# Performance work log

Hardware: AMD Instinct MI355X
Metric: run time of the kernel (lower is better)

Reference implementation:

```python
import jax, jax.numpy as jnp
from jax import lax
import numpy as np

B, S, W, Dw, Dc, F, K, Dt, P, H, T, BL = 16, 256, 16, 300, 50, 128, 3, 768, 256, 128, 9, 384
VW, VC = 100000, 128


def setup_inputs():
    ks = jax.random.split(jax.random.key(0), 32)
    f = lambda i, shape, s=0.05: jax.random.normal(ks[i], shape, dtype=jnp.float32) * s
    inp = {
        'words': jax.random.randint(ks[0], (B, S), 0, VW, dtype=jnp.int32),
        'chars': jax.random.randint(ks[1], (B, S, W), 0, VC, dtype=jnp.int32),
        'tags': jax.random.randint(ks[2], (B, S), 0, T, dtype=jnp.int32),
        'word_mask': jnp.ones((B, S), dtype=bool),
        'word_maps': jax.random.randint(ks[3], (B, S), 0, BL, dtype=jnp.int32),
        'bert_hidden': jax.random.normal(ks[4], (B, BL, Dt), dtype=jnp.float32),
        'w2v_table': f(5, (VW, Dw)).at[0].set(0.0),   # padding_idx=0
        'char_table': f(6, (VC, Dc)).at[0].set(0.0),  # padding_idx=0
        'conv_w': f(7, (F, Dc, K)), 'conv_b': f(8, (F,)),
        'w2v_pw': f(9, (Dw, P)), 'w2v_pb': f(10, (P,)),
        'char_pw': f(11, (F, P)), 'char_pb': f(12, (P,)),
        'trans_pw': f(13, (Dt, P)), 'trans_pb': f(14, (P,)),
        'attn_pw': f(15, (P, P // 2)), 'attn_pb': f(16, (P // 2,)),
        'attn_sw': f(17, (P // 2, 1)), 'attn_sb': f(18, (1,)),
        'lf_wih': f(19, (P, 4 * H)), 'lf_whh': f(20, (H, 4 * H)), 'lf_b': f(21, (4 * H,)),
        'lb_wih': f(22, (P, 4 * H)), 'lb_whh': f(23, (H, 4 * H)), 'lb_b': f(24, (4 * H,)),
        'h2t_w': f(25, (2 * H, T)), 'h2t_b': f(26, (T,)),
        'crf_start': f(27, (T,)), 'crf_end': f(28, (T,)), 'crf_trans': f(29, (T, T)),
    }
    return inp


def _lstm_dir(x, wih, whh, b, reverse):
    # x: [B,S,D]; pytorch gate order i,f,g,o; h0=c0=0
    Bx = x.shape[0]
    Hh = whh.shape[0]
    pre = jnp.einsum('bsd,dg->sbg', x, wih) + b  # [S,B,4H]
    if reverse:
        pre = pre[::-1]

    def step(carry, g):
        h, c = carry
        g = g + h @ whh
        i, f_, gg, o = jnp.split(g, 4, axis=-1)
        c = jax.nn.sigmoid(f_) * c + jax.nn.sigmoid(i) * jnp.tanh(gg)
        h = jax.nn.sigmoid(o) * jnp.tanh(c)
        return (h, c), h

    h0 = jnp.zeros((Bx, Hh), x.dtype)
    _, hs = lax.scan(step, (h0, h0), pre)
    if reverse:
        hs = hs[::-1]
    return hs.transpose(1, 0, 2)  # [B,S,H]


def _crf_loglik(emissions, tags, mask, start, end, trans):
    # torchcrf log-likelihood, batch_first inputs transposed to time-major
    Bx = emissions.shape[0]
    em = emissions.transpose(1, 0, 2)          # [S,B,T]
    tg = tags.T                                 # [S,B]
    mk = mask.T.astype(emissions.dtype)         # [S,B]
    bidx = jnp.arange(Bx)

    # numerator: score of gold path
    score0 = start[tg[0]] + em[0, bidx, tg[0]]

    def num_step(carry, x):
        score, prev = carry
        e, t, m = x
        score = score + (trans[prev, t] + e[bidx, t]) * m
        prev = jnp.where(m > 0, t, prev)
        return (score, prev), None

    (score, last_tag), _ = lax.scan(num_step, (score0, tg[0]), (em[1:], tg[1:], mk[1:]))
    numerator = score + end[last_tag]

    # denominator: forward algorithm (log-sum-exp scan)
    alpha0 = start[None, :] + em[0]

    def den_step(alpha, x):
        e, m = x
        nxt = jax.scipy.special.logsumexp(alpha[:, :, None] + trans[None] + e[:, None, :], axis=1)
        return jnp.where(m[:, None] > 0, nxt, alpha), None

    alpha, _ = lax.scan(den_step, alpha0, (em[1:], mk[1:]))
    denominator = jax.scipy.special.logsumexp(alpha + end[None, :], axis=1)
    return numerator - denominator


def reference(words, chars, tags, word_mask, word_maps, bert_hidden,
              w2v_table, char_table, conv_w, conv_b,
              w2v_pw, w2v_pb, char_pw, char_pb, trans_pw, trans_pb,
              attn_pw, attn_pb, attn_sw, attn_sb,
              lf_wih, lf_whh, lf_b, lb_wih, lb_whh, lb_b,
              h2t_w, h2t_b, crf_start, crf_end, crf_trans):
    Bx, Sx = words.shape
    w2v = w2v_table[words]                                   # [B,S,Dw]
    # CharCNN: embed -> conv1d (same pad) -> max over word_len
    ce = char_table[chars]                                   # [B,S,W,Dc]
    x = ce.reshape(Bx * Sx, ce.shape[2], ce.shape[3]).transpose(0, 2, 1)  # [BS,Dc,W]
    k = conv_w.shape[-1]
    c = lax.conv_general_dilated(x, conv_w, (1,), [(k // 2, k // 2)],
                                 dimension_numbers=('NCW', 'OIW', 'NCW'))
    c = c + conv_b[None, :, None]
    char_feat = c.max(axis=2).reshape(Bx, Sx, -1)            # [B,S,F]
    # gather subword states to word positions (vectorized word_maps double-loop)
    tf = jnp.take_along_axis(bert_hidden, word_maps[:, :, None], axis=1)  # [B,S,Dt]
    p1 = jax.nn.relu(w2v @ w2v_pw + w2v_pb)
    p2 = jax.nn.relu(char_feat @ char_pw + char_pb)
    p3 = jax.nn.relu(tf @ trans_pw + trans_pb)
    stacked = jnp.stack([p1, p2, p3], axis=2)                # [B,S,3,P]
    proj = jnp.tanh(stacked @ attn_pw + attn_pb)
    scores = (proj @ attn_sw + attn_sb)[..., 0]              # [B,S,3]
    wts = jax.nn.softmax(scores, axis=2)
    fused = (wts[..., None] * stacked).sum(axis=2)           # [B,S,P]
    hf = _lstm_dir(fused, lf_wih, lf_whh, lf_b, False)
    hb = _lstm_dir(fused, lb_wih, lb_whh, lb_b, True)
    lstm_out = jnp.concatenate([hf, hb], axis=-1)            # [B,S,2H]
    emissions = lstm_out @ h2t_w + h2t_b                     # [B,S,T]
    llh = _crf_loglik(emissions, tags, word_mask, crf_start, crf_end, crf_trans)
    return -llh.mean()
```

## Files before the change

### kernel.cpp

```cpp
#include <hip/hip_runtime.h>
#include <math.h>

#define BB   16
#define SS   256
#define WWID 16
#define DW   300
#define DC   50
#define FF   128
#define DT   768
#define PP   256
#define HH   128
#define TT   9
#define BLL  384
#define NTOK (BB*SS)

__device__ __forceinline__ float sigmoidf_(float x){ return 1.f/(1.f+expf(-x)); }
__device__ __forceinline__ float fsig_(float x){ return __frcp_rn(1.f + __expf(-x)); }
__device__ __forceinline__ float ftanh_(float x){ return 1.f - 2.f*__frcp_rn(__expf(2.f*x) + 1.f); }

__global__ void k_charconv(const int* __restrict__ chars,
                           const float* __restrict__ char_table,
                           const float* __restrict__ conv_w,
                           const float* __restrict__ conv_b,
                           float* __restrict__ char_feat){
  __shared__ __align__(16) float sm_ce[WWID][DC];
  const int tok = blockIdx.x;
  const int tid = threadIdx.x;
  for (int idx = tid; idx < WWID*DC; idx += 128){
    int w = idx / DC, c = idx - w*DC;
    sm_ce[w][c] = char_table[chars[tok*WWID + w]*DC + c];
  }
  __syncthreads();
  const int f = tid;
  float acc[WWID];
  const float bias = conv_b[f];
  #pragma unroll
  for (int w = 0; w < WWID; w++) acc[w] = bias;
  const float* cw = conv_w + f*DC*3;
  for (int c = 0; c < DC; c++){
    float w0 = cw[c*3+0], w1 = cw[c*3+1], w2 = cw[c*3+2];
    float xm = 0.f, x0 = sm_ce[0][c];
    #pragma unroll
    for (int w = 0; w < WWID; w++){
      float xp = (w < WWID-1) ? sm_ce[w+1][c] : 0.f;
      acc[w] += xm*w0 + x0*w1 + xp*w2;
      xm = x0; x0 = xp;
    }
  }
  float mx = acc[0];
  #pragma unroll
  for (int w = 1; w < WWID; w++) mx = fmaxf(mx, acc[w]);
  char_feat[tok*FF + f] = mx;
}

__global__ void k_proj(const int* __restrict__ words,
                       const int* __restrict__ word_maps,
                       const float* __restrict__ w2v_table,
                       const float* __restrict__ bert,
                       const float* __restrict__ char_feat,
                       const float* __restrict__ w2v_pw, const float* __restrict__ w2v_pb,
                       const float* __restrict__ char_pw, const float* __restrict__ char_pb,
                       const float* __restrict__ trans_pw, const float* __restrict__ trans_pb,
                       float* __restrict__ stacked){
  const int MT = 16;
  __shared__ __align__(16) float sm_x[MT*128];
  const int bx  = blockIdx.x;
  const int src = bx >> 8;
  const int m0  = (bx & 255) * MT;
  const int tid = threadIdx.x;
  const int Ksz = (src==0) ? DW : (src==1 ? FF : DT);
  const float* Wt = (src==0) ? w2v_pw : (src==1 ? char_pw : trans_pw);
  const float* bv = (src==0) ? w2v_pb : (src==1 ? char_pb : trans_pb);

  float acc[MT];
  #pragma unroll
  for (int m = 0; m < MT; m++) acc[m] = 0.f;

  for (int kc = 0; kc < Ksz; kc += 128){
    const int kk = min(128, Ksz - kc);
    for (int m = 0; m < MT; m++){
      const int tok = m0 + m;
      for (int k = tid; k < kk; k += 256){
        float v;
        if (src == 0)      v = w2v_table[(long)words[tok]*DW + kc + k];
        else if (src == 1) v = char_feat[tok*FF + kc + k];
        else               v = bert[((long)(tok>>8)*BLL + word_maps[tok])*DT + kc + k];
        sm_x[m*128 + k] = v;
      }
    }
    __syncthreads();
    const int k4 = kk & ~3;
    for (int k = 0; k < k4; k += 4){
      const float wv0 = Wt[(kc+k+0)*PP + tid];
      const float wv1 = Wt[(kc+k+1)*PP + tid];
      const float wv2 = Wt[(kc+k+2)*PP + tid];
      const float wv3 = Wt[(kc+k+3)*PP + tid];
      #pragma unroll
      for (int m = 0; m < MT; m++){
        const float4 x = *reinterpret_cast<const float4*>(&sm_x[m*128 + k]);
        acc[m] += x.x*wv0 + x.y*wv1 + x.z*wv2 + x.w*wv3;
      }
    }
    for (int k = k4; k < kk; k++){
      const float wv = Wt[(kc+k)*PP + tid];
      #pragma unroll
      for (int m = 0; m < MT; m++) acc[m] += sm_x[m*128 + k]*wv;
    }
    __syncthreads();
  }
  const float b0 = bv[tid];
  for (int m = 0; m < MT; m++){
    const float v = fmaxf(acc[m] + b0, 0.f);
    stacked[((long)(m0+m)*3 + src)*PP + tid] = v;
  }
}

__global__ void k_attn(const float* __restrict__ stacked,
                       const float* __restrict__ attn_pw, const float* __restrict__ attn_pb,
                       const float* __restrict__ attn_sw, const float* __restrict__ attn_sb,
                       float* __restrict__ fused){
  const int MT = 4;
  __shared__ __align__(16) float sm_st[MT*3*PP];
  __shared__ float sm_prod[MT*3*128];
  __shared__ float sm_sc[MT*3];
  __shared__ float sm_w[MT][3];
  const int m0  = blockIdx.x * MT;
  const int tid = threadIdx.x;
  for (int idx = tid; idx < MT*3*PP; idx += 256)
    sm_st[idx] = stacked[(long)m0*3*PP + idx];
  __syncthreads();
  for (int task = tid; task < MT*3*128; task += 256){
    const int i = task / 384;
    const int r = task - i*384;
    const int j = r >> 7;
    const int q = r & 127;
    const float* xv = &sm_st[(i*3 + j)*PP];
    float acc = attn_pb[q];
    for (int p = 0; p < PP; p += 4){
      const float4 x = *reinterpret_cast<const float4*>(&xv[p]);
      acc += x.x*attn_pw[(p+0)*128+q] + x.y*attn_pw[(p+1)*128+q]
           + x.z*attn_pw[(p+2)*128+q] + x.w*attn_pw[(p+3)*128+q];
    }
    sm_prod[task] = tanhf(acc) * attn_sw[q];
  }
  __syncthreads();
  if (tid < MT*3){
    const int i = tid/3, j = tid - i*3;
    float s = attn_sb[0];
    for (int q = 0; q < 128; q++) s += sm_prod[(i*3 + j)*128 + q];
    sm_sc[tid] = s;
  }
  __syncthreads();
  if (tid < MT){
    const float a = sm_sc[tid*3], b = sm_sc[tid*3+1], c = sm_sc[tid*3+2];
    const float m = fmaxf(a, fmaxf(b, c));
    const float ea = expf(a-m), eb = expf(b-m), ec = expf(c-m);
    const float inv = 1.f/(ea+eb+ec);
    sm_w[tid][0] = ea*inv; sm_w[tid][1] = eb*inv; sm_w[tid][2] = ec*inv;
  }
  __syncthreads();
  for (int idx = tid; idx < MT*PP; idx += 256){
    const int i = idx >> 8, p = idx & 255;
    const float v = sm_w[i][0]*sm_st[(i*3+0)*PP+p]
                  + sm_w[i][1]*sm_st[(i*3+1)*PP+p]
                  + sm_w[i][2]*sm_st[(i*3+2)*PP+p];
    fused[(long)(m0+i)*PP + p] = v;
  }
}

__global__ void k_pre(const float* __restrict__ fused,
                      const float* __restrict__ lf_wih, const float* __restrict__ lf_b,
                      const float* __restrict__ lb_wih, const float* __restrict__ lb_b,
                      float* __restrict__ pre_f, float* __restrict__ pre_b){
  const int MT = 8;
  __shared__ __align__(16) float sm_f[MT*PP];
  const int m0  = blockIdx.x * MT;
  const int tid = threadIdx.x;
  for (int idx = tid; idx < MT*PP; idx += 512) sm_f[idx] = fused[(long)m0*PP + idx];
  __syncthreads();
  float af[MT], ab[MT];
  #pragma unroll
  for (int m = 0; m < MT; m++){ af[m] = 0.f; ab[m] = 0.f; }
  for (int k = 0; k < PP; k += 4){
    const float wf0 = lf_wih[(k+0)*512 + tid];
    const float wf1 = lf_wih[(k+1)*512 + tid];
    const float wf2 = lf_wih[(k+2)*512 + tid];
    const float wf3 = lf_wih[(k+3)*512 + tid];
    const float wb0 = lb_wih[(k+0)*512 + tid];
    const float wb1 = lb_wih[(k+1)*512 + tid];
    const float wb2 = lb_wih[(k+2)*512 + tid];
    const float wb3 = lb_wih[(k+3)*512 + tid];
    #pragma unroll
    for (int m = 0; m < MT; m++){
      const float4 x = *reinterpret_cast<const float4*>(&sm_f[m*PP + k]);
      af[m] += x.x*wf0 + x.y*wf1 + x.z*wf2 + x.w*wf3;
      ab[m] += x.x*wb0 + x.y*wb1 + x.z*wb2 + x.w*wb3;
    }
  }
  const float bf = lf_b[tid], bbv = lb_b[tid];
  for (int m = 0; m < MT; m++){
    pre_f[(long)(m0+m)*512 + tid] = af[m] + bf;
    pre_b[(long)(m0+m)*512 + tid] = ab[m] + bbv;
  }
}

#define LDW(i) float4 W##i; \
  W##i.x = wcol[(4*(i)+0)*512]; W##i.y = wcol[(4*(i)+1)*512]; \
  W##i.z = wcol[(4*(i)+2)*512]; W##i.w = wcol[(4*(i)+3)*512];
#define FMW(i) { const float4 h4 = *reinterpret_cast<const float4*>(&sm_h[4*(i)]); \
  g0 = fmaf(h4.x, W##i.x, g0); g1 = fmaf(h4.y, W##i.y, g1); \
  g2 = fmaf(h4.z, W##i.z, g2); g3 = fmaf(h4.w, W##i.w, g3); }

__global__ void __launch_bounds__(512, 1)
k_lstm(const float* __restrict__ pre_f, const float* __restrict__ pre_b,
       const float* __restrict__ lf_whh, const float* __restrict__ lb_whh,
       float* __restrict__ lstm_out){
  __shared__ __align__(16) float sm_h[HH];
  __shared__ __align__(16) float sm_g[512];
  const int b = blockIdx.x & 15;
  const int d = blockIdx.x >> 4;
  const float* pre = d ? pre_b : pre_f;
  const float* whh = d ? lb_whh : lf_whh;
  const int tid = threadIdx.x;

  const float* wcol = whh + tid;
  LDW(0)  LDW(1)  LDW(2)  LDW(3)  LDW(4)  LDW(5)  LDW(6)  LDW(7)
  LDW(8)  LDW(9)  LDW(10) LDW(11) LDW(12) LDW(13) LDW(14) LDW(15)
  LDW(16) LDW(17) LDW(18) LDW(19) LDW(20) LDW(21) LDW(22) LDW(23)
  LDW(24) LDW(25) LDW(26) LDW(27) LDW(28) LDW(29) LDW(30) LDW(31)

  float c = 0.f;
  if (tid < HH) sm_h[tid] = 0.f;
  __syncthreads();

  const long step = d ? -512 : 512;
  const float* pp = pre + ((long)b*SS + (d ? SS-1 : 0))*512 + tid;
  float pcur = *pp;

  for (int s = 0; s < SS; s++){
    const int ss = d ? (SS-1-s) : s;
    pp += step;
    float pnext = (s+1 < SS) ? *pp : 0.f;
    float g0 = pcur, g1 = 0.f, g2 = 0.f, g3 = 0.f;
    FMW(0)  FMW(1)  FMW(2)  FMW(3)  FMW(4)  FMW(5)  FMW(6)  FMW(7)
    FMW(8)  FMW(9)  FMW(10) FMW(11) FMW(12) FMW(13) FMW(14) FMW(15)
    FMW(16) FMW(17) FMW(18) FMW(19) FMW(20) FMW(21) FMW(22) FMW(23)
    FMW(24) FMW(25) FMW(26) FMW(27) FMW(28) FMW(29) FMW(30) FMW(31)
    sm_g[tid] = (g0+g1)+(g2+g3);
    __syncthreads();
    if (tid < HH){
      const float iv = fsig_(sm_g[tid]);
      const float fv = fsig_(sm_g[HH + tid]);
      const float gv = ftanh_(sm_g[2*HH + tid]);
      const float ov = fsig_(sm_g[3*HH + tid]);
      c = fv*c + iv*gv;
      const float h = ov*ftanh_(c);
      sm_h[tid] = h;
      lstm_out[((long)b*SS + ss)*(2*HH) + d*HH + tid] = h;
    }
    __syncthreads();
    pcur = pnext;
  }
}

__global__ void k_emis(const float* __restrict__ lstm_out,
                       const float* __restrict__ h2t_w, const float* __restrict__ h2t_b,
                       float* __restrict__ emis){
  const int idx = blockIdx.x*blockDim.x + threadIdx.x;
  if (idx >= NTOK*TT) return;
  const int tok = idx / TT, t = idx - tok*TT;
  float acc = h2t_b[t];
  const float* x = &lstm_out[(long)tok*256];
  for (int k = 0; k < 256; k++) acc += x[k]*h2t_w[k*TT + t];
  emis[idx] = acc;
}

__global__ void k_crf(const float* __restrict__ emis, const int* __restrict__ tags,
                      const float* __restrict__ startv, const float* __restrict__ endv,
                      const float* __restrict__ trans, float* __restrict__ out){
  __shared__ float sm_part[256];
  __shared__ float sm_num[BB];
  __shared__ float sm_den[BB];
  __shared__ float sm_a[2][BB][TT+3];
  const int tid = threadIdx.x;
  {
    const int b = tid >> 4, part = tid & 15;
    float ps = 0.f;
    for (int s = part; s < SS; s += 16){
      const int tg = tags[b*SS + s];
      ps += emis[((long)b*SS + s)*TT + tg];
      if (s > 0) ps += trans[tags[b*SS + s - 1]*TT + tg];
    }
    if (part == 0) ps += startv[tags[b*SS]] + endv[tags[b*SS + SS - 1]];
    sm_part[tid] = ps;
  }
  __syncthreads();
  if (tid < BB){
    float s = 0.f;
    for (int i = 0; i < 16; i++) s += sm_part[tid*16 + i];
    sm_num[tid] = s;
  }
  const int ab = tid / TT, at = tid - ab*TT;
  if (tid < BB*TT)
    sm_a[0][ab][at] = startv[at] + emis[((long)ab*SS)*TT + at];
  __syncthreads();
  float trC[TT];
  if (tid < BB*TT){
    #pragma unroll
    for (int p = 0; p < TT; p++) trC[p] = trans[p*TT + at];
  }
  int cur = 0;
  for (int s = 1; s < SS; s++){
    if (tid < BB*TT){
      float av[TT], m = -1e30f;
      #pragma unroll
      for (int p = 0; p < TT; p++){ av[p] = sm_a[cur][ab][p] + trC[p]; m = fmaxf(m, av[p]); }
      float sum = 0.f;
      #pragma unroll
      for (int p = 0; p < TT; p++) sum += expf(av[p] - m);
      sm_a[1-cur][ab][at] = m + logf(sum) + emis[((long)ab*SS + s)*TT + at];
    }
    __syncthreads();
    cur ^= 1;
  }
  if (tid < BB){
    float av[TT], m = -1e30f;
    #pragma unroll
    for (int t2 = 0; t2 < TT; t2++){ av[t2] = sm_a[cur][tid][t2] + endv[t2]; m = fmaxf(m, av[t2]); }
    float sum = 0.f;
    #pragma unroll
    for (int t2 = 0; t2 < TT; t2++) sum += expf(av[t2] - m);
    sm_den[tid] = m + logf(sum);
  }
  __syncthreads();
  if (tid == 0){
    float acc = 0.f;
    for (int i = 0; i < BB; i++) acc += sm_num[i] - sm_den[i];
    out[0] = -acc / (float)BB;
  }
}

extern "C" void kernel_launch(void* const* d_in, const int* in_sizes, int n_in,
                              void* d_out, int out_size, void* d_ws, size_t ws_size,
                              hipStream_t stream) {
  const int*   words      = (const int*)  d_in[0];
  const int*   chars      = (const int*)  d_in[1];
  const int*   tags       = (const int*)  d_in[2];
  const int*   word_maps  = (const int*)  d_in[4];
  const float* bert       = (const float*)d_in[5];
  const float* w2v_table  = (const float*)d_in[6];
  const float* char_table = (const float*)d_in[7];
  const float* conv_w     = (const float*)d_in[8];
  const float* conv_b     = (const float*)d_in[9];
  const float* w2v_pw     = (const float*)d_in[10];
  const float* w2v_pb     = (const float*)d_in[11];
  const float* char_pw    = (const float*)d_in[12];
  const float* char_pb    = (const float*)d_in[13];
  const float* trans_pw   = (const float*)d_in[14];
  const float* trans_pb   = (const float*)d_in[15];
  const float* attn_pw    = (const float*)d_in[16];
  const float* attn_pb    = (const float*)d_in[17];
  const float* attn_sw    = (const float*)d_in[18];
  const float* attn_sb    = (const float*)d_in[19];
  const float* lf_wih     = (const float*)d_in[20];
  const float* lf_whh     = (const float*)d_in[21];
  const float* lf_b       = (const float*)d_in[22];
  const float* lb_wih     = (const float*)d_in[23];
  const float* lb_whh     = (const float*)d_in[24];
  const float* lb_b       = (const float*)d_in[25];
  const float* h2t_w      = (const float*)d_in[26];
  const float* h2t_b      = (const float*)d_in[27];
  const float* crf_start  = (const float*)d_in[28];
  const float* crf_end    = (const float*)d_in[29];
  const float* crf_trans  = (const float*)d_in[30];
  float* outp = (float*)d_out;

  float* char_feat = (float*)d_ws;
  float* stacked   = char_feat + (long)NTOK*FF;
  float* fused     = stacked   + (long)NTOK*3*PP;
  float* pre_f     = fused     + (long)NTOK*PP;
  float* pre_b     = pre_f     + (long)NTOK*512;
  float* lstm_out  = pre_b     + (long)NTOK*512;
  float* emis      = lstm_out  + (long)NTOK*256;

  k_charconv<<<NTOK, 128, 0, stream>>>(chars, char_table, conv_w, conv_b, char_feat);
  k_proj<<<3*256, 256, 0, stream>>>(words, word_maps, w2v_table, bert, char_feat,
                                    w2v_pw, w2v_pb, char_pw, char_pb, trans_pw, trans_pb,
                                    stacked);
  k_attn<<<NTOK/4, 256, 0, stream>>>(stacked, attn_pw, attn_pb, attn_sw, attn_sb, fused);
  k_pre<<<NTOK/8, 512, 0, stream>>>(fused, lf_wih, lf_b, lb_wih, lb_b, pre_f, pre_b);
  k_lstm<<<32, 512, 0, stream>>>(pre_f, pre_b, lf_whh, lb_whh, lstm_out);
  k_emis<<<(NTOK*TT + 255)/256, 256, 0, stream>>>(lstm_out, h2t_w, h2t_b, emis);
  k_crf<<<1, 256, 0, stream>>>(emis, tags, crf_start, crf_end, crf_trans, outp);
}
```

Measured before the change: 1.013 ms.

## Pack LSTM recurrent weights to fp16 pairs in LDS and use dot2 accumulation

A new pre-pass kernel converts the recurrent weight matrices to packed fp16 pairs. The LSTM kernel stages these into a 128KB LDS buffer and does the recurrence with fdot2 over fp16 hidden-state pairs, instead of holding 128 fp32 weights per thread in registers. This halves the FMA count on the serial path and frees registers, but it adds an LDS read per dot2 and loses precision in the weights and the hidden state.

```diff
diff --git a/kernel.cpp b/kernel.cpp
--- a/kernel.cpp
+++ b/kernel.cpp
@@ -1,4 +1,5 @@
 #include <hip/hip_runtime.h>
+#include <hip/hip_fp16.h>
 #include <math.h>
 
 #define BB   16
@@ -17,6 +18,19 @@
 __device__ __forceinline__ float sigmoidf_(float x){ return 1.f/(1.f+expf(-x)); }
 __device__ __forceinline__ float fsig_(float x){ return __frcp_rn(1.f + __expf(-x)); }
 __device__ __forceinline__ float ftanh_(float x){ return 1.f - 2.f*__frcp_rn(__expf(2.f*x) + 1.f); }
+
+typedef _Float16 h2_t __attribute__((ext_vector_type(2)));
+union U32H2 { unsigned u; h2_t h; };
+
+__device__ __forceinline__ float dot2f(unsigned a, unsigned b, float c){
+  U32H2 ua; ua.u = a;
+  U32H2 ub; ub.u = b;
+#if __has_builtin(__builtin_amdgcn_fdot2)
+  return __builtin_amdgcn_fdot2(ua.h, ub.h, c, false);
+#else
+  return c + (float)ua.h[0]*(float)ub.h[0] + (float)ua.h[1]*(float)ub.h[1];
+#endif
+}
 
 __global__ void k_charconv(const int* __restrict__ chars,
                            const float* __restrict__ char_table,
@@ -204,33 +218,39 @@
   }
 }
 
-#define LDW(i) float4 W##i; \
-  W##i.x = wcol[(4*(i)+0)*512]; W##i.y = wcol[(4*(i)+1)*512]; \
-  W##i.z = wcol[(4*(i)+2)*512]; W##i.w = wcol[(4*(i)+3)*512];
-#define FMW(i) { const float4 h4 = *reinterpret_cast<const float4*>(&sm_h[4*(i)]); \
-  g0 = fmaf(h4.x, W##i.x, g0); g1 = fmaf(h4.y, W##i.y, g1); \
-  g2 = fmaf(h4.z, W##i.z, g2); g3 = fmaf(h4.w, W##i.w, g3); }
+__global__ void k_packw(const float* __restrict__ lf_whh, const float* __restrict__ lb_whh,
+                        unsigned* __restrict__ wpk){
+  const int idx = blockIdx.x*256 + threadIdx.x;
+  if (idx >= 2*64*512) return;
+  const int d   = idx >> 15;
+  const int r   = idx & 32767;
+  const int j   = r >> 9;
+  const int col = r & 511;
+  const float* w = d ? lb_whh : lf_whh;
+  const float a = w[(2*j)*512 + col];
+  const float b = w[(2*j+1)*512 + col];
+  U32H2 p; p.h = h2_t{(_Float16)a, (_Float16)b};
+  wpk[idx] = p.u;
+}
 
 __global__ void __launch_bounds__(512, 1)
 k_lstm(const float* __restrict__ pre_f, const float* __restrict__ pre_b,
-       const float* __restrict__ lf_whh, const float* __restrict__ lb_whh,
+       const unsigned* __restrict__ wpk,
        float* __restrict__ lstm_out){
-  __shared__ __align__(16) float sm_h[HH];
-  __shared__ __align__(16) float sm_g[512];
+  __shared__ unsigned w_lds[64*512];
+  __shared__ __align__(16) unsigned sm_hp[64];
+  __shared__ float sm_g[512];
   const int b = blockIdx.x & 15;
   const int d = blockIdx.x >> 4;
   const float* pre = d ? pre_b : pre_f;
-  const float* whh = d ? lb_whh : lf_whh;
-  const int tid = threadIdx.x;
-
-  const float* wcol = whh + tid;
-  LDW(0)  LDW(1)  LDW(2)  LDW(3)  LDW(4)  LDW(5)  LDW(6)  LDW(7)
-  LDW(8)  LDW(9)  LDW(10) LDW(11) LDW(12) LDW(13) LDW(14) LDW(15)
-  LDW(16) LDW(17) LDW(18) LDW(19) LDW(20) LDW(21) LDW(22) LDW(23)
-  LDW(24) LDW(25) LDW(26) LDW(27) LDW(28) LDW(29) LDW(30) LDW(31)
+  const int tid = threadIdx.x;
+
+  const unsigned* wsrc = wpk + (long)d*64*512;
+  #pragma unroll
+  for (int i = 0; i < 64; i++) w_lds[i*512 + tid] = wsrc[i*512 + tid];
 
   float c = 0.f;
-  if (tid < HH) sm_h[tid] = 0.f;
+  if (tid < 64) sm_hp[tid] = 0u;
   __syncthreads();
 
   const long step = d ? -512 : 512;
@@ -242,10 +262,15 @@
     pp += step;
     float pnext = (s+1 < SS) ? *pp : 0.f;
     float g0 = pcur, g1 = 0.f, g2 = 0.f, g3 = 0.f;
-    FMW(0)  FMW(1)  FMW(2)  FMW(3)  FMW(4)  FMW(5)  FMW(6)  FMW(7)
-    FMW(8)  FMW(9)  FMW(10) FMW(11) FMW(12) FMW(13) FMW(14) FMW(15)
-    FMW(16) FMW(17) FMW(18) FMW(19) FMW(20) FMW(21) FMW(22) FMW(23)
-    FMW(24) FMW(25) FMW(26) FMW(27) FMW(28) FMW(29) FMW(30) FMW(31)
+    const unsigned* wrow = w_lds + tid;
+    #pragma unroll
+    for (int j = 0; j < 64; j += 4){
+      const uint4 hp = *reinterpret_cast<const uint4*>(&sm_hp[j]);
+      g0 = dot2f(hp.x, wrow[(j+0)*512], g0);
+      g1 = dot2f(hp.y, wrow[(j+1)*512], g1);
+      g2 = dot2f(hp.z, wrow[(j+2)*512], g2);
+      g3 = dot2f(hp.w, wrow[(j+3)*512], g3);
+    }
     sm_g[tid] = (g0+g1)+(g2+g3);
     __syncthreads();
     if (tid < HH){
@@ -255,8 +280,12 @@
       const float ov = fsig_(sm_g[3*HH + tid]);
       c = fv*c + iv*gv;
       const float h = ov*ftanh_(c);
-      sm_h[tid] = h;
       lstm_out[((long)b*SS + ss)*(2*HH) + d*HH + tid] = h;
+      const float hn = __shfl_down(h, 1);
+      if ((tid & 1) == 0){
+        U32H2 p; p.h = h2_t{(_Float16)h, (_Float16)hn};
+        sm_hp[tid >> 1] = p.u;
+      }
     }
     __syncthreads();
     pcur = pnext;
@@ -382,14 +411,16 @@
   float* pre_b     = pre_f     + (long)NTOK*512;
   float* lstm_out  = pre_b     + (long)NTOK*512;
   float* emis      = lstm_out  + (long)NTOK*256;
+  unsigned* wpk    = (unsigned*)(emis + (long)NTOK*TT);
 
   k_charconv<<<NTOK, 128, 0, stream>>>(chars, char_table, conv_w, conv_b, char_feat);
+  k_packw<<<256, 256, 0, stream>>>(lf_whh, lb_whh, wpk);
   k_proj<<<3*256, 256, 0, stream>>>(words, word_maps, w2v_table, bert, char_feat,
                                     w2v_pw, w2v_pb, char_pw, char_pb, trans_pw, trans_pb,
                                     stacked);
   k_attn<<<NTOK/4, 256, 0, stream>>>(stacked, attn_pw, attn_pb, attn_sw, attn_sb, fused);
   k_pre<<<NTOK/8, 512, 0, stream>>>(fused, lf_wih, lf_b, lb_wih, lb_b, pre_f, pre_b);
-  k_lstm<<<32, 512, 0, stream>>>(pre_f, pre_b, lf_whh, lb_whh, lstm_out);
+  k_lstm<<<32, 512, 0, stream>>>(pre_f, pre_b, wpk, lstm_out);
   k_emis<<<(NTOK*TT + 255)/256, 256, 0, stream>>>(lstm_out, h2t_w, h2t_b, emis);
   k_crf<<<1, 256, 0, stream>>>(emis, tags, crf_start, crf_end, crf_trans, outp);
 }
```

Result: faster. 958.1 us (-5.4%).
